# Performance work log

Hardware: AMD Instinct MI355X
Metric: run time of the kernel (lower is better)

Reference implementation:

```python
import jax, jax.numpy as jnp
import numpy as np

B, N, H = 8, 256, 128
EPS = 1e-5

def setup_inputs() -> dict:
    key = jax.random.key(0)
    ks = jax.random.split(key, 16)
    s = 1.0 / np.sqrt(H)
    inp = {
        "x": jax.random.normal(ks[0], (B, N, H), jnp.float32),
        "e": jax.random.normal(ks[1], (B, N, N, H), jnp.float32),
        # EdgeFeatures: U, V linear layers
        "Ue_w": jax.random.normal(ks[2], (H, H), jnp.float32) * s,
        "Ue_b": jax.random.normal(ks[3], (H,), jnp.float32) * s,
        "Ve_w": jax.random.normal(ks[4], (H, H), jnp.float32) * s,
        "Ve_b": jax.random.normal(ks[5], (H,), jnp.float32) * s,
        # NodeFeatures: U, V linear layers
        "Un_w": jax.random.normal(ks[6], (H, H), jnp.float32) * s,
        "Un_b": jax.random.normal(ks[7], (H,), jnp.float32) * s,
        "Vn_w": jax.random.normal(ks[8], (H, H), jnp.float32) * s,
        "Vn_b": jax.random.normal(ks[9], (H,), jnp.float32) * s,
        # BatchNorm affine params (track_running_stats=False -> batch stats)
        "bne_w": jnp.ones((H,), jnp.float32),
        "bne_b": jnp.zeros((H,), jnp.float32),
        "bnn_w": jnp.ones((H,), jnp.float32),
        "bnn_b": jnp.zeros((H,), jnp.float32),
    }
    return inp

def _bn(t, axes, w, b):
    # BatchNorm with batch statistics (biased variance), per-channel over last dim
    m = jnp.mean(t, axis=axes, keepdims=True)
    v = jnp.var(t, axis=axes, keepdims=True)
    return (t - m) * jax.lax.rsqrt(v + EPS) * w + b

def reference(x, e, Ue_w, Ue_b, Ve_w, Ve_b, Un_w, Un_b, Vn_w, Vn_b,
              bne_w, bne_b, bnn_w, bnn_b):
    # EdgeFeatures: e_new = U(e) + V(x)_i + V(x)_j  -> [B,N,N,H]
    Vx = x @ Ve_w.T + Ve_b                              # [B,N,H]
    e_new = e @ Ue_w.T + Ue_b + Vx[:, :, None, :] + Vx[:, None, :, :]
    gate = jax.nn.sigmoid(e_new)                        # [B,N,N,H]
    # NodeFeatures (aggregation='sum'): Ux + sum_j gate_ij * Vn(x)_j
    Vnx = x @ Vn_w.T + Vn_b                             # [B,N,H]
    agg = jnp.sum(gate * Vnx[:, None, :, :], axis=2)    # [B,N,H]
    x_new = x @ Un_w.T + Un_b + agg
    # BatchNorm (batch stats) + ReLU + residual
    e_bn = _bn(e_new, (0, 1, 2), bne_w, bne_b)
    x_bn = _bn(x_new, (0, 1), bnn_w, bnn_b)
    return x + jax.nn.relu(x_bn), e + jax.nn.relu(e_bn)
```

## Files before the change

### kernel.cpp

```cpp
#include <hip/hip_runtime.h>
#include <cstdint>
#include <cstddef>


typedef float  f4v  __attribute__((ext_vector_type(4)));
typedef short  s8v  __attribute__((ext_vector_type(8)));

__device__ __forceinline__ unsigned short f2bf(float x) {
    unsigned u = __builtin_bit_cast(unsigned, x);
    u = (u + 0x7FFFu + ((u >> 16) & 1u)) >> 16;
    return (unsigned short)u;
}

__device__ __forceinline__ float sigmoid_f(float v) {
    float e = exp2f(-1.44269504088896f * v);
    return __builtin_amdgcn_rcpf(1.0f + e);
}

__global__ __launch_bounds__(256) void k0_proj(
    const float* __restrict__ x,
    const float* __restrict__ Ve_w, const float* __restrict__ Ve_b,
    const float* __restrict__ Vn_w, const float* __restrict__ Vn_b,
    const float* __restrict__ Un_w, const float* __restrict__ Un_b,
    const float* __restrict__ Ue_w,
    float* __restrict__ ws)
{
    int bid = blockIdx.x;
    int tid = threadIdx.x;

    if (bid >= 768) {
        int g = (bid - 768) * 256 + tid;
        const float4* src = (const float4*)(Ue_w + g * 16);
        unsigned short* Wbf = (unsigned short*)(ws + 1049600);
        float4 v0 = src[0], v1 = src[1], v2 = src[2], v3 = src[3];
        s8v p0, p1;
        p0[0] = (short)f2bf(v0.x); p0[1] = (short)f2bf(v0.y);
        p0[2] = (short)f2bf(v0.z); p0[3] = (short)f2bf(v0.w);
        p0[4] = (short)f2bf(v1.x); p0[5] = (short)f2bf(v1.y);
        p0[6] = (short)f2bf(v1.z); p0[7] = (short)f2bf(v1.w);
        p1[0] = (short)f2bf(v2.x); p1[1] = (short)f2bf(v2.y);
        p1[2] = (short)f2bf(v2.z); p1[3] = (short)f2bf(v2.w);
        p1[4] = (short)f2bf(v3.x); p1[5] = (short)f2bf(v3.y);
        p1[6] = (short)f2bf(v3.z); p1[7] = (short)f2bf(v3.w);
        *(s8v*)(Wbf + g * 16)     = p0;
        *(s8v*)(Wbf + g * 16 + 8) = p1;
        return;
    }

    int m = bid >> 8;
    int rbase = (bid & 255) * 8;
    int h = tid & 127;
    int lr = tid >> 7;

    const float* W; const float* bb; float* out;
    if (m == 0)      { W = Ve_w; bb = Ve_b; out = ws; }
    else if (m == 1) { W = Vn_w; bb = Vn_b; out = ws + 262144; }
    else             { W = Un_w; bb = Un_b; out = ws + 524288; }

    __shared__ __align__(16) float xs[8][128];
    for (int idx = tid; idx < 1024; idx += 256)
        xs[idx >> 7][idx & 127] = x[(rbase + (idx >> 7)) * 128 + (idx & 127)];

    if (bid == 0) {
        ws[1048576 + tid] = 0.0f;
        ws[1048576 + 256 + tid] = 0.0f;
    }
    __syncthreads();

    float acc[4] = {0.f, 0.f, 0.f, 0.f};
    float bv = bb[h];
    const float4* Wr = (const float4*)(W + h * 128);
    for (int k4 = 0; k4 < 32; ++k4) {
        float4 w4 = Wr[k4];
        int k = k4 * 4;
        #pragma unroll
        for (int q = 0; q < 4; ++q) {
            int rl = lr * 4 + q;
            acc[q] += w4.x * xs[rl][k] + w4.y * xs[rl][k + 1]
                    + w4.z * xs[rl][k + 2] + w4.w * xs[rl][k + 3];
        }
    }
    #pragma unroll
    for (int q = 0; q < 4; ++q)
        out[(rbase + lr * 4 + q) * 128 + h] = acc[q] + bv;
}

__global__ __launch_bounds__(256, 4) void k1_stats(
    const float* __restrict__ e,
    const float* __restrict__ Ue_b,
    float* __restrict__ ws)
{
    const float* Vx  = ws;
    const float* Vnx = ws + 262144;
    const float* Ux  = ws + 524288;
    float* agg    = ws + 786432;
    float* esum   = ws + 1048576;
    float* esumsq = ws + 1048704;
    float* nsum   = ws + 1048832;
    float* nsumsq = ws + 1048960;
    const unsigned short* Wbf = (const unsigned short*)(ws + 1049600);

    int bid = blockIdx.x;
    int b = bid >> 8;
    int tid = threadIdx.x;
    int wave = tid >> 6;
    int lane = tid & 63;
    int col  = lane & 15;
    int quad = lane >> 4;
    int h0 = wave * 32 + col;
    int h1 = h0 + 16;

    __shared__ __align__(16) unsigned short Al[2][32 * 136];
    __shared__ float addi[128];

    if (tid < 128) addi[tid] = Ue_b[tid] + Vx[bid * 128 + tid];

    s8v wf0[4], wf1[4];
    #pragma unroll
    for (int kk = 0; kk < 4; ++kk) {
        wf0[kk] = *(const s8v*)(Wbf + h0 * 128 + kk * 32 + quad * 8);
        wf1[kk] = *(const s8v*)(Wbf + h1 * 128 + kk * 32 + quad * 8);
    }

    const int arow = tid >> 4;
    const int akb  = (tid & 15) * 8;
    const float* eblk = e + (size_t)bid * 32768;

    float4 pv0, pv1, pv2, pv3;
    {
        const float4* s0 = (const float4*)(eblk + arow * 128 + akb);
        const float4* s1 = (const float4*)(eblk + (arow + 16) * 128 + akb);
        pv0 = s0[0]; pv1 = s0[1]; pv2 = s1[0]; pv3 = s1[1];
    }

    float sum0 = 0.f, sum1 = 0.f, ss0 = 0.f, ss1 = 0.f, ag0 = 0.f, ag1 = 0.f;

    for (int jt = 0; jt < 8; ++jt) {
        unsigned short* Ac = &Al[jt & 1][0];
        {
            s8v pa, pb;
            pa[0] = (short)f2bf(pv0.x); pa[1] = (short)f2bf(pv0.y);
            pa[2] = (short)f2bf(pv0.z); pa[3] = (short)f2bf(pv0.w);
            pa[4] = (short)f2bf(pv1.x); pa[5] = (short)f2bf(pv1.y);
            pa[6] = (short)f2bf(pv1.z); pa[7] = (short)f2bf(pv1.w);
            pb[0] = (short)f2bf(pv2.x); pb[1] = (short)f2bf(pv2.y);
            pb[2] = (short)f2bf(pv2.z); pb[3] = (short)f2bf(pv2.w);
            pb[4] = (short)f2bf(pv3.x); pb[5] = (short)f2bf(pv3.y);
            pb[6] = (short)f2bf(pv3.z); pb[7] = (short)f2bf(pv3.w);
            *(s8v*)(&Ac[arow * 136 + akb])        = pa;
            *(s8v*)(&Ac[(arow + 16) * 136 + akb]) = pb;
        }
        if (jt < 7) {
            const float4* s0 = (const float4*)(eblk + ((jt + 1) * 32 + arow) * 128 + akb);
            const float4* s1 = (const float4*)(eblk + ((jt + 1) * 32 + arow + 16) * 128 + akb);
            pv0 = s0[0]; pv1 = s0[1]; pv2 = s1[0]; pv3 = s1[1];
        }
        asm volatile("s_waitcnt lgkmcnt(0)" ::: "memory");
        __builtin_amdgcn_s_barrier();

        #pragma unroll
        for (int js = 0; js < 2; ++js) {
            f4v acc0 = {0.f, 0.f, 0.f, 0.f}, acc1 = {0.f, 0.f, 0.f, 0.f};
            #pragma unroll
            for (int kk = 0; kk < 4; ++kk) {
                s8v a = *(const s8v*)(&Ac[(js * 16 + col) * 136 + kk * 32 + quad * 8]);
                acc0 = __builtin_amdgcn_mfma_f32_16x16x32_bf16(a, wf0[kk], acc0, 0, 0, 0);
                acc1 = __builtin_amdgcn_mfma_f32_16x16x32_bf16(a, wf1[kk], acc1, 0, 0, 0);
            }
            float ai0 = addi[h0], ai1 = addi[h1];
            #pragma unroll
            for (int r = 0; r < 4; ++r) {
                int j = jt * 32 + js * 16 + quad * 4 + r;
                const float* vxr = Vx  + (size_t)((b << 8) + j) * 128;
                const float* vnr = Vnx + (size_t)((b << 8) + j) * 128;
                float v0 = acc0[r] + ai0 + vxr[h0];
                float v1 = acc1[r] + ai1 + vxr[h1];
                sum0 += v0; ss0 += v0 * v0;
                sum1 += v1; ss1 += v1 * v1;
                ag0 += sigmoid_f(v0) * vnr[h0];
                ag1 += sigmoid_f(v1) * vnr[h1];
            }
        }
    }

    sum0 += __shfl_xor(sum0, 16); sum0 += __shfl_xor(sum0, 32);
    sum1 += __shfl_xor(sum1, 16); sum1 += __shfl_xor(sum1, 32);
    ss0  += __shfl_xor(ss0, 16);  ss0  += __shfl_xor(ss0, 32);
    ss1  += __shfl_xor(ss1, 16);  ss1  += __shfl_xor(ss1, 32);
    ag0  += __shfl_xor(ag0, 16);  ag0  += __shfl_xor(ag0, 32);
    ag1  += __shfl_xor(ag1, 16);  ag1  += __shfl_xor(ag1, 32);

    if (lane < 16) {
        atomicAdd(&esum[h0], sum0);
        atomicAdd(&esumsq[h0], ss0);
        atomicAdd(&esum[h1], sum1);
        atomicAdd(&esumsq[h1], ss1);
        agg[bid * 128 + h0] = ag0;
        agg[bid * 128 + h1] = ag1;
        float v0 = Ux[bid * 128 + h0] + ag0;
        float v1 = Ux[bid * 128 + h1] + ag1;
        atomicAdd(&nsum[h0], v0);
        atomicAdd(&nsumsq[h0], v0 * v0);
        atomicAdd(&nsum[h1], v1);
        atomicAdd(&nsumsq[h1], v1 * v1);
    }
}

__global__ __launch_bounds__(256, 4) void k2_apply(
    const float* __restrict__ e,
    const float* __restrict__ x,
    const float* __restrict__ Ue_b,
    const float* __restrict__ bne_w, const float* __restrict__ bne_b,
    const float* __restrict__ bnn_w, const float* __restrict__ bnn_b,
    const float* __restrict__ ws, float* __restrict__ out_x,
    float* __restrict__ out_e)
{
    const float* Vx   = ws;
    const float* Ux   = ws + 524288;
    const float* agg  = ws + 786432;
    const float* esum = ws + 1048576;
    const float* esumsq = ws + 1048704;
    const float* nsum = ws + 1048832;
    const float* nsumsq = ws + 1048960;
    const unsigned short* Wbf = (const unsigned short*)(ws + 1049600);

    int bid = blockIdx.x;
    int b = bid >> 8;
    int tid = threadIdx.x;
    int wave = tid >> 6;
    int lane = tid & 63;
    int col  = lane & 15;
    int quad = lane >> 4;
    int h0 = wave * 32 + col;
    int h1 = h0 + 16;

    __shared__ __align__(16) unsigned short Al[2][32 * 136];
    __shared__ float addi[128], escl[128], eshl[128];

    if (tid < 128) {
        float m  = esum[tid]   * (1.0f / 524288.0f);
        float q  = esumsq[tid] * (1.0f / 524288.0f);
        float rs = rsqrtf(q - m * m + 1e-5f);
        float sc = rs * bne_w[tid];
        escl[tid] = sc;
        eshl[tid] = bne_b[tid] - m * sc;
        addi[tid] = Ue_b[tid] + Vx[bid * 128 + tid];

        float mn  = nsum[tid]   * (1.0f / 2048.0f);
        float qn  = nsumsq[tid] * (1.0f / 2048.0f);
        float rsn = rsqrtf(qn - mn * mn + 1e-5f);
        float scn = rsn * bnn_w[tid];
        float shn = bnn_b[tid] - mn * scn;
        float v = Ux[bid * 128 + tid] + agg[bid * 128 + tid];
        out_x[bid * 128 + tid] = x[bid * 128 + tid] + fmaxf(v * scn + shn, 0.0f);
    }

    s8v wf0[4], wf1[4];
    #pragma unroll
    for (int kk = 0; kk < 4; ++kk) {
        wf0[kk] = *(const s8v*)(Wbf + h0 * 128 + kk * 32 + quad * 8);
        wf1[kk] = *(const s8v*)(Wbf + h1 * 128 + kk * 32 + quad * 8);
    }

    const int arow = tid >> 4;
    const int akb  = (tid & 15) * 8;
    const float* eblk = e + (size_t)bid * 32768;
    float* oblk = out_e + (size_t)bid * 32768;

    float4 pv0, pv1, pv2, pv3;
    {
        const float4* s0 = (const float4*)(eblk + arow * 128 + akb);
        const float4* s1 = (const float4*)(eblk + (arow + 16) * 128 + akb);
        pv0 = s0[0]; pv1 = s0[1]; pv2 = s1[0]; pv3 = s1[1];
    }

    for (int jt = 0; jt < 8; ++jt) {
        unsigned short* Ac = &Al[jt & 1][0];
        {
            s8v pa, pb;
            pa[0] = (short)f2bf(pv0.x); pa[1] = (short)f2bf(pv0.y);
            pa[2] = (short)f2bf(pv0.z); pa[3] = (short)f2bf(pv0.w);
            pa[4] = (short)f2bf(pv1.x); pa[5] = (short)f2bf(pv1.y);
            pa[6] = (short)f2bf(pv1.z); pa[7] = (short)f2bf(pv1.w);
            pb[0] = (short)f2bf(pv2.x); pb[1] = (short)f2bf(pv2.y);
            pb[2] = (short)f2bf(pv2.z); pb[3] = (short)f2bf(pv2.w);
            pb[4] = (short)f2bf(pv3.x); pb[5] = (short)f2bf(pv3.y);
            pb[6] = (short)f2bf(pv3.z); pb[7] = (short)f2bf(pv3.w);
            *(s8v*)(&Ac[arow * 136 + akb])        = pa;
            *(s8v*)(&Ac[(arow + 16) * 136 + akb]) = pb;
        }
        if (jt < 7) {
            const float4* s0 = (const float4*)(eblk + ((jt + 1) * 32 + arow) * 128 + akb);
            const float4* s1 = (const float4*)(eblk + ((jt + 1) * 32 + arow + 16) * 128 + akb);
            pv0 = s0[0]; pv1 = s0[1]; pv2 = s1[0]; pv3 = s1[1];
        }
        asm volatile("s_waitcnt lgkmcnt(0)" ::: "memory");
        __builtin_amdgcn_s_barrier();

        #pragma unroll
        for (int js = 0; js < 2; ++js) {
            f4v acc0 = {0.f, 0.f, 0.f, 0.f}, acc1 = {0.f, 0.f, 0.f, 0.f};
            #pragma unroll
            for (int kk = 0; kk < 4; ++kk) {
                s8v a = *(const s8v*)(&Ac[(js * 16 + col) * 136 + kk * 32 + quad * 8]);
                acc0 = __builtin_amdgcn_mfma_f32_16x16x32_bf16(a, wf0[kk], acc0, 0, 0, 0);
                acc1 = __builtin_amdgcn_mfma_f32_16x16x32_bf16(a, wf1[kk], acc1, 0, 0, 0);
            }
            float ai0 = addi[h0], ai1 = addi[h1];
            float sc0 = escl[h0], sh0 = eshl[h0];
            float sc1 = escl[h1], sh1 = eshl[h1];
            #pragma unroll
            for (int r = 0; r < 4; ++r) {
                int j = jt * 32 + js * 16 + quad * 4 + r;
                const float* vxr = Vx + (size_t)((b << 8) + j) * 128;
                float v0 = acc0[r] + ai0 + vxr[h0];
                float v1 = acc1[r] + ai1 + vxr[h1];
                float r0 = fmaxf(v0 * sc0 + sh0, 0.0f);
                float r1 = fmaxf(v1 * sc1 + sh1, 0.0f);
                oblk[j * 128 + h0] = eblk[j * 128 + h0] + r0;
                oblk[j * 128 + h1] = eblk[j * 128 + h1] + r1;
            }
        }
    }
}

extern "C" void kernel_launch(void* const* d_in, const int* in_sizes, int n_in,
                              void* d_out, int out_size, void* d_ws, size_t ws_size,
                              hipStream_t stream)
{
    const float* x     = (const float*)d_in[0];
    const float* e     = (const float*)d_in[1];
    const float* Ue_w  = (const float*)d_in[2];
    const float* Ue_b  = (const float*)d_in[3];
    const float* Ve_w  = (const float*)d_in[4];
    const float* Ve_b  = (const float*)d_in[5];
    const float* Un_w  = (const float*)d_in[6];
    const float* Un_b  = (const float*)d_in[7];
    const float* Vn_w  = (const float*)d_in[8];
    const float* Vn_b  = (const float*)d_in[9];
    const float* bne_w = (const float*)d_in[10];
    const float* bne_b = (const float*)d_in[11];
    const float* bnn_w = (const float*)d_in[12];
    const float* bnn_b = (const float*)d_in[13];
    float* ws    = (float*)d_ws;
    float* out_x = (float*)d_out;
    float* out_e = (float*)d_out + 262144;

    hipLaunchKernelGGL(k0_proj, dim3(772), dim3(256), 0, stream,
                       x, Ve_w, Ve_b, Vn_w, Vn_b, Un_w, Un_b, Ue_w, ws);
    hipLaunchKernelGGL(k1_stats, dim3(2048), dim3(256), 0, stream,
                       e, Ue_b, ws);
    hipLaunchKernelGGL(k2_apply, dim3(2048), dim3(256), 0, stream,
                       e, x, Ue_b, bne_w, bne_b, bnn_w, bnn_b, ws, out_x, out_e);
}
```

Baseline: 583.0 us.

## Load MFMA A-fragments directly from global memory, dropping the LDS staging

After: 744.7 us. +27.7%, slower.

```diff
diff --git a/kernel.cpp b/kernel.cpp
--- a/kernel.cpp
+++ b/kernel.cpp
@@ -10,6 +10,21 @@
     unsigned u = __builtin_bit_cast(unsigned, x);
     u = (u + 0x7FFFu + ((u >> 16) & 1u)) >> 16;
     return (unsigned short)u;
+}
+
+__device__ __forceinline__ unsigned cvtpk(float lo, float hi) {
+    unsigned r;
+    asm("v_cvt_pk_bf16_f32 %0, %1, %2" : "=v"(r) : "v"(lo), "v"(hi));
+    return r;
+}
+
+__device__ __forceinline__ s8v pack8(float4 a, float4 b) {
+    union { unsigned u[4]; s8v v; } r;
+    r.u[0] = cvtpk(a.x, a.y);
+    r.u[1] = cvtpk(a.z, a.w);
+    r.u[2] = cvtpk(b.x, b.y);
+    r.u[3] = cvtpk(b.z, b.w);
+    return r.v;
 }
 
 __device__ __forceinline__ float sigmoid_f(float v) {
@@ -33,15 +48,8 @@
         const float4* src = (const float4*)(Ue_w + g * 16);
         unsigned short* Wbf = (unsigned short*)(ws + 1049600);
         float4 v0 = src[0], v1 = src[1], v2 = src[2], v3 = src[3];
-        s8v p0, p1;
-        p0[0] = (short)f2bf(v0.x); p0[1] = (short)f2bf(v0.y);
-        p0[2] = (short)f2bf(v0.z); p0[3] = (short)f2bf(v0.w);
-        p0[4] = (short)f2bf(v1.x); p0[5] = (short)f2bf(v1.y);
-        p0[6] = (short)f2bf(v1.z); p0[7] = (short)f2bf(v1.w);
-        p1[0] = (short)f2bf(v2.x); p1[1] = (short)f2bf(v2.y);
-        p1[2] = (short)f2bf(v2.z); p1[3] = (short)f2bf(v2.w);
-        p1[4] = (short)f2bf(v3.x); p1[5] = (short)f2bf(v3.y);
-        p1[6] = (short)f2bf(v3.z); p1[7] = (short)f2bf(v3.w);
+        s8v p0 = pack8(v0, v1);
+        s8v p1 = pack8(v2, v3);
         *(s8v*)(Wbf + g * 16)     = p0;
         *(s8v*)(Wbf + g * 16 + 8) = p1;
         return;
@@ -110,9 +118,7 @@
     int h0 = wave * 32 + col;
     int h1 = h0 + 16;
 
-    __shared__ __align__(16) unsigned short Al[2][32 * 136];
     __shared__ float addi[128];
-
     if (tid < 128) addi[tid] = Ue_b[tid] + Vx[bid * 128 + tid];
 
     s8v wf0[4], wf1[4];
@@ -121,65 +127,45 @@
         wf0[kk] = *(const s8v*)(Wbf + h0 * 128 + kk * 32 + quad * 8);
         wf1[kk] = *(const s8v*)(Wbf + h1 * 128 + kk * 32 + quad * 8);
     }
-
-    const int arow = tid >> 4;
-    const int akb  = (tid & 15) * 8;
+    __syncthreads();
+    float ai0 = addi[h0], ai1 = addi[h1];
+
     const float* eblk = e + (size_t)bid * 32768;
 
-    float4 pv0, pv1, pv2, pv3;
-    {
-        const float4* s0 = (const float4*)(eblk + arow * 128 + akb);
-        const float4* s1 = (const float4*)(eblk + (arow + 16) * 128 + akb);
-        pv0 = s0[0]; pv1 = s0[1]; pv2 = s1[0]; pv3 = s1[1];
-    }
-
     float sum0 = 0.f, sum1 = 0.f, ss0 = 0.f, ss1 = 0.f, ag0 = 0.f, ag1 = 0.f;
 
-    for (int jt = 0; jt < 8; ++jt) {
-        unsigned short* Ac = &Al[jt & 1][0];
-        {
-            s8v pa, pb;
-            pa[0] = (short)f2bf(pv0.x); pa[1] = (short)f2bf(pv0.y);
-            pa[2] = (short)f2bf(pv0.z); pa[3] = (short)f2bf(pv0.w);
-            pa[4] = (short)f2bf(pv1.x); pa[5] = (short)f2bf(pv1.y);
-            pa[6] = (short)f2bf(pv1.z); pa[7] = (short)f2bf(pv1.w);
-            pb[0] = (short)f2bf(pv2.x); pb[1] = (short)f2bf(pv2.y);
-            pb[2] = (short)f2bf(pv2.z); pb[3] = (short)f2bf(pv2.w);
-            pb[4] = (short)f2bf(pv3.x); pb[5] = (short)f2bf(pv3.y);
-            pb[6] = (short)f2bf(pv3.z); pb[7] = (short)f2bf(pv3.w);
-            *(s8v*)(&Ac[arow * 136 + akb])        = pa;
-            *(s8v*)(&Ac[(arow + 16) * 136 + akb]) = pb;
-        }
-        if (jt < 7) {
-            const float4* s0 = (const float4*)(eblk + ((jt + 1) * 32 + arow) * 128 + akb);
-            const float4* s1 = (const float4*)(eblk + ((jt + 1) * 32 + arow + 16) * 128 + akb);
-            pv0 = s0[0]; pv1 = s0[1]; pv2 = s1[0]; pv3 = s1[1];
-        }
-        asm volatile("s_waitcnt lgkmcnt(0)" ::: "memory");
-        __builtin_amdgcn_s_barrier();
+    for (int js = 0; js < 16; ++js) {
+        const float4* er = (const float4*)(eblk + (size_t)(js * 16 + col) * 128) + quad * 2;
+        float4 c0 = er[0],  c1 = er[1];
+        float4 c2 = er[8],  c3 = er[9];
+        float4 c4 = er[16], c5 = er[17];
+        float4 c6 = er[24], c7 = er[25];
+        s8v a0 = pack8(c0, c1);
+        s8v a1 = pack8(c2, c3);
+        s8v a2 = pack8(c4, c5);
+        s8v a3 = pack8(c6, c7);
+
+        f4v acc0 = {0.f, 0.f, 0.f, 0.f}, acc1 = {0.f, 0.f, 0.f, 0.f};
+        acc0 = __builtin_amdgcn_mfma_f32_16x16x32_bf16(a0, wf0[0], acc0, 0, 0, 0);
+        acc1 = __builtin_amdgcn_mfma_f32_16x16x32_bf16(a0, wf1[0], acc1, 0, 0, 0);
+        acc0 = __builtin_amdgcn_mfma_f32_16x16x32_bf16(a1, wf0[1], acc0, 0, 0, 0);
+        acc1 = __builtin_amdgcn_mfma_f32_16x16x32_bf16(a1, wf1[1], acc1, 0, 0, 0);
+        acc0 = __builtin_amdgcn_mfma_f32_16x16x32_bf16(a2, wf0[2], acc0, 0, 0, 0);
+        acc1 = __builtin_amdgcn_mfma_f32_16x16x32_bf16(a2, wf1[2], acc1, 0, 0, 0);
+        acc0 = __builtin_amdgcn_mfma_f32_16x16x32_bf16(a3, wf0[3], acc0, 0, 0, 0);
+        acc1 = __builtin_amdgcn_mfma_f32_16x16x32_bf16(a3, wf1[3], acc1, 0, 0, 0);
 
         #pragma unroll
-        for (int js = 0; js < 2; ++js) {
-            f4v acc0 = {0.f, 0.f, 0.f, 0.f}, acc1 = {0.f, 0.f, 0.f, 0.f};
-            #pragma unroll
-            for (int kk = 0; kk < 4; ++kk) {
-                s8v a = *(const s8v*)(&Ac[(js * 16 + col) * 136 + kk * 32 + quad * 8]);
-                acc0 = __builtin_amdgcn_mfma_f32_16x16x32_bf16(a, wf0[kk], acc0, 0, 0, 0);
-                acc1 = __builtin_amdgcn_mfma_f32_16x16x32_bf16(a, wf1[kk], acc1, 0, 0, 0);
-            }
-            float ai0 = addi[h0], ai1 = addi[h1];
-            #pragma unroll
-            for (int r = 0; r < 4; ++r) {
-                int j = jt * 32 + js * 16 + quad * 4 + r;
-                const float* vxr = Vx  + (size_t)((b << 8) + j) * 128;
-                const float* vnr = Vnx + (size_t)((b << 8) + j) * 128;
-                float v0 = acc0[r] + ai0 + vxr[h0];
-                float v1 = acc1[r] + ai1 + vxr[h1];
-                sum0 += v0; ss0 += v0 * v0;
-                sum1 += v1; ss1 += v1 * v1;
-                ag0 += sigmoid_f(v0) * vnr[h0];
-                ag1 += sigmoid_f(v1) * vnr[h1];
-            }
+        for (int r = 0; r < 4; ++r) {
+            int j = js * 16 + quad * 4 + r;
+            const float* vxr = Vx  + (size_t)((b << 8) + j) * 128;
+            const float* vnr = Vnx + (size_t)((b << 8) + j) * 128;
+            float v0 = acc0[r] + ai0 + vxr[h0];
+            float v1 = acc1[r] + ai1 + vxr[h1];
+            sum0 += v0; ss0 += v0 * v0;
+            sum1 += v1; ss1 += v1 * v1;
+            ag0 += sigmoid_f(v0) * vnr[h0];
+            ag1 += sigmoid_f(v1) * vnr[h1];
         }
     }
 
@@ -234,7 +220,6 @@
     int h0 = wave * 32 + col;
     int h1 = h0 + 16;
 
-    __shared__ __align__(16) unsigned short Al[2][32 * 136];
     __shared__ float addi[128], escl[128], eshl[128];
 
     if (tid < 128) {
@@ -261,65 +246,45 @@
         wf0[kk] = *(const s8v*)(Wbf + h0 * 128 + kk * 32 + quad * 8);
         wf1[kk] = *(const s8v*)(Wbf + h1 * 128 + kk * 32 + quad * 8);
     }
-
-    const int arow = tid >> 4;
-    const int akb  = (tid & 15) * 8;
+    __syncthreads();
+    float ai0 = addi[h0], ai1 = addi[h1];
+    float sc0 = escl[h0], sh0 = eshl[h0];
+    float sc1 = escl[h1], sh1 = eshl[h1];
+
     const float* eblk = e + (size_t)bid * 32768;
     float* oblk = out_e + (size_t)bid * 32768;
 
-    float4 pv0, pv1, pv2, pv3;
-    {
-        const float4* s0 = (const float4*)(eblk + arow * 128 + akb);
-        const float4* s1 = (const float4*)(eblk + (arow + 16) * 128 + akb);
-        pv0 = s0[0]; pv1 = s0[1]; pv2 = s1[0]; pv3 = s1[1];
-    }
-
-    for (int jt = 0; jt < 8; ++jt) {
-        unsigned short* Ac = &Al[jt & 1][0];
-        {
-            s8v pa, pb;
-            pa[0] = (short)f2bf(pv0.x); pa[1] = (short)f2bf(pv0.y);
-            pa[2] = (short)f2bf(pv0.z); pa[3] = (short)f2bf(pv0.w);
-            pa[4] = (short)f2bf(pv1.x); pa[5] = (short)f2bf(pv1.y);
-            pa[6] = (short)f2bf(pv1.z); pa[7] = (short)f2bf(pv1.w);
-            pb[0] = (short)f2bf(pv2.x); pb[1] = (short)f2bf(pv2.y);
-            pb[2] = (short)f2bf(pv2.z); pb[3] = (short)f2bf(pv2.w);
-            pb[4] = (short)f2bf(pv3.x); pb[5] = (short)f2bf(pv3.y);
-            pb[6] = (short)f2bf(pv3.z); pb[7] = (short)f2bf(pv3.w);
-            *(s8v*)(&Ac[arow * 136 + akb])        = pa;
-            *(s8v*)(&Ac[(arow + 16) * 136 + akb]) = pb;
-        }
-        if (jt < 7) {
-            const float4* s0 = (const float4*)(eblk + ((jt + 1) * 32 + arow) * 128 + akb);
-            const float4* s1 = (const float4*)(eblk + ((jt + 1) * 32 + arow + 16) * 128 + akb);
-            pv0 = s0[0]; pv1 = s0[1]; pv2 = s1[0]; pv3 = s1[1];
-        }
-        asm volatile("s_waitcnt lgkmcnt(0)" ::: "memory");
-        __builtin_amdgcn_s_barrier();
+    for (int js = 0; js < 16; ++js) {
+        const float4* er = (const float4*)(eblk + (size_t)(js * 16 + col) * 128) + quad * 2;
+        float4 c0 = er[0],  c1 = er[1];
+        float4 c2 = er[8],  c3 = er[9];
+        float4 c4 = er[16], c5 = er[17];
+        float4 c6 = er[24], c7 = er[25];
+        s8v a0 = pack8(c0, c1);
+        s8v a1 = pack8(c2, c3);
+        s8v a2 = pack8(c4, c5);
+        s8v a3 = pack8(c6, c7);
+
+        f4v acc0 = {0.f, 0.f, 0.f, 0.f}, acc1 = {0.f, 0.f, 0.f, 0.f};
+        acc0 = __builtin_amdgcn_mfma_f32_16x16x32_bf16(a0, wf0[0], acc0, 0, 0, 0);
+        acc1 = __builtin_amdgcn_mfma_f32_16x16x32_bf16(a0, wf1[0], acc1, 0, 0, 0);
+        acc0 = __builtin_amdgcn_mfma_f32_16x16x32_bf16(a1, wf0[1], acc0, 0, 0, 0);
+        acc1 = __builtin_amdgcn_mfma_f32_16x16x32_bf16(a1, wf1[1], acc1, 0, 0, 0);
+        acc0 = __builtin_amdgcn_mfma_f32_16x16x32_bf16(a2, wf0[2], acc0, 0, 0, 0);
+        acc1 = __builtin_amdgcn_mfma_f32_16x16x32_bf16(a2, wf1[2], acc1, 0, 0, 0);
+        acc0 = __builtin_amdgcn_mfma_f32_16x16x32_bf16(a3, wf0[3], acc0, 0, 0, 0);
+        acc1 = __builtin_amdgcn_mfma_f32_16x16x32_bf16(a3, wf1[3], acc1, 0, 0, 0);
 
         #pragma unroll
-        for (int js = 0; js < 2; ++js) {
-            f4v acc0 = {0.f, 0.f, 0.f, 0.f}, acc1 = {0.f, 0.f, 0.f, 0.f};
-            #pragma unroll
-            for (int kk = 0; kk < 4; ++kk) {
-                s8v a = *(const s8v*)(&Ac[(js * 16 + col) * 136 + kk * 32 + quad * 8]);
-                acc0 = __builtin_amdgcn_mfma_f32_16x16x32_bf16(a, wf0[kk], acc0, 0, 0, 0);
-                acc1 = __builtin_amdgcn_mfma_f32_16x16x32_bf16(a, wf1[kk], acc1, 0, 0, 0);
-            }
-            float ai0 = addi[h0], ai1 = addi[h1];
-            float sc0 = escl[h0], sh0 = eshl[h0];
-            float sc1 = escl[h1], sh1 = eshl[h1];
-            #pragma unroll
-            for (int r = 0; r < 4; ++r) {
-                int j = jt * 32 + js * 16 + quad * 4 + r;
-                const float* vxr = Vx + (size_t)((b << 8) + j) * 128;
-                float v0 = acc0[r] + ai0 + vxr[h0];
-                float v1 = acc1[r] + ai1 + vxr[h1];
-                float r0 = fmaxf(v0 * sc0 + sh0, 0.0f);
-                float r1 = fmaxf(v1 * sc1 + sh1, 0.0f);
-                oblk[j * 128 + h0] = eblk[j * 128 + h0] + r0;
-                oblk[j * 128 + h1] = eblk[j * 128 + h1] + r1;
-            }
+        for (int r = 0; r < 4; ++r) {
+            int j = js * 16 + quad * 4 + r;
+            const float* vxr = Vx + (size_t)((b << 8) + j) * 128;
+            float v0 = acc0[r] + ai0 + vxr[h0];
+            float v1 = acc1[r] + ai1 + vxr[h1];
+            float r0 = fmaxf(v0 * sc0 + sh0, 0.0f);
+            float r1 = fmaxf(v1 * sc1 + sh1, 0.0f);
+            oblk[(size_t)j * 128 + h0] = eblk[(size_t)j * 128 + h0] + r0;
+            oblk[(size_t)j * 128 + h1] = eblk[(size_t)j * 128 + h1] + r1;
         }
     }
 }
```
